# Kernel tuning notes

Hardware: AMD Instinct MI355X
Metric: run time of the kernel (lower is better)

The kernel has to match this reference:

```python
import jax, jax.numpy as jnp
import numpy as np

B, L, D, H = 4, 1024, 1024, 16
HD = D // H            # head dim 64
MAXP = 1024            # max_position_embeddings
NADJ = 2               # teacher layers mapped to this student layer


def setup_inputs() -> dict:
    key = jax.random.key(0)
    ks = jax.random.split(key, 6)
    return {
        "hidden_states": jax.random.normal(ks[0], (B, L, D), jnp.float32),
        "attention_mask": jnp.zeros((B, 1, 1, L), jnp.float32),
        "teacher_w": jax.random.normal(ks[1], (3, NADJ, D, D), jnp.float32) * 0.02,
        "wl_w": jax.random.normal(ks[2], (3, NADJ), jnp.float32),
        "scale_w": jnp.ones((3, D, D), jnp.float32),
        "shift_w": jnp.zeros((3, D, D), jnp.float32),
        "teacher_b": jax.random.normal(ks[3], (3, NADJ, D), jnp.float32) * 0.02,
        "wl_b": jax.random.normal(ks[4], (3, NADJ), jnp.float32),
        "scale_b": jnp.ones((3, D), jnp.float32),
        "shift_b": jnp.zeros((3, D), jnp.float32),
        "dist_emb": jax.random.normal(ks[5], (2 * MAXP - 1, HD), jnp.float32) * 0.02,
    }


def reference(hidden_states, attention_mask, teacher_w, wl_w, scale_w, shift_w,
              teacher_b, wl_b, scale_b, shift_b, dist_emb):
    # Teacher-distilled weight/bias generation (WeightGenerator/BiasGenerator):
    # student = tanh(mode-0 contraction of teacher subset with W_l) * W + B
    w = jnp.tanh(jnp.einsum('pl,ploi->poi', wl_w, teacher_w)) * scale_w + shift_w  # [3,out,in]
    b = jnp.tanh(jnp.einsum('pl,plo->po', wl_b, teacher_b)) * scale_b + shift_b    # [3,out]

    def proj(i):
        y = jnp.einsum('bld,od->blo', hidden_states, w[i]) + b[i]
        return y.reshape(B, L, H, HD).transpose(0, 2, 1, 3)  # [B,H,L,HD]

    q, k, v = proj(0), proj(1), proj(2)

    scores = jnp.einsum('bhld,bhrd->bhlr', q, k)  # [B,H,L,L]

    # relative_key_query positional bias
    dist = jnp.arange(L)[:, None] - jnp.arange(L)[None, :] + (MAXP - 1)  # [L,L]
    pe = dist_emb[dist]                                                  # [L,L,HD]
    scores = scores \
        + jnp.einsum('bhld,lrd->bhlr', q, pe) \
        + jnp.einsum('bhrd,lrd->bhlr', k, pe)

    scores = scores / np.sqrt(HD).astype(np.float32) + attention_mask
    probs = jax.nn.softmax(scores, axis=-1)  # dropout p=0.0 (eval)

    ctx = jnp.einsum('bhlr,bhrd->bhld', probs, v)
    return ctx.transpose(0, 2, 1, 3).reshape(B, L, D)
```

## Files before the change

kernel.cpp:

```cpp
#include <hip/hip_runtime.h>
#include <hip/hip_bf16.h>
#include <math.h>

#define D_  1024
#define L_  1024
#define B_  4
#define H_  16
#define HD_ 64

typedef __attribute__((ext_vector_type(4))) short short4_t;
typedef __attribute__((ext_vector_type(8))) short short8_t;
typedef __attribute__((ext_vector_type(4))) float f4;
typedef unsigned short u16;

__device__ __forceinline__ f4 MF(short8_t a, short8_t b, f4 c) {
  return __builtin_amdgcn_mfma_f32_16x16x32_bf16(a, b, c, 0, 0, 0);
}
__device__ __forceinline__ unsigned fbits(float x) { return __builtin_bit_cast(unsigned, x); }
__device__ __forceinline__ float bf2f(unsigned short u) {
  return __builtin_bit_cast(float, (unsigned)u << 16);
}
__device__ __forceinline__ unsigned pack2hi(float x, float y) {
  return (fbits(x) >> 16) | (fbits(y) & 0xFFFF0000u);
}
__device__ __forceinline__ float bfres(float x) {
  return x - __builtin_bit_cast(float, fbits(x) & 0xFFFF0000u);
}
__device__ __forceinline__ void gload16(const void* g, void* l) {
  __builtin_amdgcn_global_load_lds(
      (const __attribute__((address_space(1))) unsigned*)g,
      (__attribute__((address_space(3))) unsigned*)l, 16, 0, 0);
}
__device__ __forceinline__ short8_t ldsfragP(const char* base, int row, int ci) {
  return *(const short8_t*)(base + row * 128 + ((ci ^ (row & 7)) << 4));
}
__device__ __forceinline__ int perm32(int c) {
  return (c & ~31) | (((c >> 2) & 3) << 3) | (((c >> 4) & 1) << 2);
}

__global__ __launch_bounds__(256) void wgen_kernel(
    const float* __restrict__ tw, const float* __restrict__ wl,
    const float* __restrict__ sc, const float* __restrict__ sh,
    u16* __restrict__ whi, u16* __restrict__ wlo) {
  size_t i4 = (size_t)blockIdx.x * 256 + threadIdx.x;
  size_t e = i4 * 4;
  int p = (int)(e >> 20);
  size_t rem = e & 0xFFFFFu;
  float a0 = wl[p * 2 + 0], a1 = wl[p * 2 + 1];
  float4 t0 = *(const float4*)&tw[((size_t)(p * 2 + 0) << 20) + rem];
  float4 t1 = *(const float4*)&tw[((size_t)(p * 2 + 1) << 20) + rem];
  float4 s4 = *(const float4*)&sc[e];
  float4 h4 = *(const float4*)&sh[e];
  float4 o;
  o.x = tanhf(a0 * t0.x + a1 * t1.x) * s4.x + h4.x;
  o.y = tanhf(a0 * t0.y + a1 * t1.y) * s4.y + h4.y;
  o.z = tanhf(a0 * t0.z + a1 * t1.z) * s4.z + h4.z;
  o.w = tanhf(a0 * t0.w + a1 * t1.w) * s4.w + h4.w;
  const size_t off = (e & ~(size_t)1023) + perm32((int)(e & 1023) & 31) +
                     (((int)(e & 1023)) & ~31);
  uint2 hi; hi.x = pack2hi(o.x, o.y); hi.y = pack2hi(o.z, o.w);
  *(uint2*)&whi[off] = hi;
  uint2 lo; lo.x = pack2hi(bfres(o.x), bfres(o.y)); lo.y = pack2hi(bfres(o.z), bfres(o.w));
  *(uint2*)&wlo[off] = lo;
}

__global__ __launch_bounds__(256) void bgen_kernel(
    const float* __restrict__ tb, const float* __restrict__ wl,
    const float* __restrict__ sc, const float* __restrict__ sh,
    float* __restrict__ b_out) {
  int i = blockIdx.x * 256 + threadIdx.x;
  int p = i >> 10;
  int o = i & 1023;
  float v = tanhf(wl[p * 2 + 0] * tb[(p * 2 + 0) * D_ + o] +
                  wl[p * 2 + 1] * tb[(p * 2 + 1) * D_ + o]);
  b_out[i] = v * sc[i] + sh[i];
}

__global__ __launch_bounds__(256) void ecvt_kernel(
    const float* __restrict__ emb, u16* __restrict__ embh) {
  int i4 = blockIdx.x * 256 + threadIdx.x;
  if (i4 >= 32752) return;
  int e = i4 * 4;
  float4 v = *(const float4*)&emb[e];
  uint2 h2; h2.x = pack2hi(v.x, v.y); h2.y = pack2hi(v.z, v.w);
  int pe = (e & ~31) | perm32(e & 31);
  *(uint2*)&embh[pe] = h2;
}

__global__ __launch_bounds__(256) void proj_mfma_kernel(
    const float* __restrict__ hs,
    const u16* __restrict__ Bhp, const u16* __restrict__ Blp,
    const float* __restrict__ bias,
    u16* __restrict__ Qhi, u16* __restrict__ Qlo,
    u16* __restrict__ Khi, u16* __restrict__ Klo,
    u16* __restrict__ Vthi, u16* __restrict__ Vtlo) {
  __shared__ u16 Ah[128][32], Al[128][32], Bh[128][32], Bl[128][32];
  const int tid  = threadIdx.x;
  const int lane = tid & 63;
  const int wv   = tid >> 6;
  const int wm   = wv >> 1, wn = wv & 1;
  const int l15  = lane & 15, g = lane >> 4;

  const int bid = (blockIdx.x & 7) * 96 + (blockIdx.x >> 3);
  const int mt = bid & 31, nt = bid >> 5;
  const int m0 = mt * 128, n0 = nt * 128;

  f4 acc[4][4];
#pragma unroll
  for (int i = 0; i < 4; ++i)
#pragma unroll
    for (int j = 0; j < 4; ++j) acc[i][j] = f4{0.f, 0.f, 0.f, 0.f};

#pragma unroll 1
  for (int k0 = 0; k0 < D_; k0 += 32) {
#pragma unroll
    for (int s = 0; s < 4; ++s) {
      int q = wv * 4 + s;
      int plane = q >> 3, rowg = q & 7;
      const u16* src = (plane ? Blp : Bhp) +
                       (size_t)(n0 + rowg * 16 + (lane >> 2)) * 1024 + k0 + (lane & 3) * 8;
      u16* dst = (plane ? &Bl[0][0] : &Bh[0][0]) + rowg * 512;
      gload16(src, dst);
    }
#pragma unroll
    for (int c = 0; c < 4; ++c) {
      int f4id = tid + c * 256;
      int row = f4id >> 3, q4 = f4id & 7;
      float4 v = *(const float4*)&hs[(size_t)(m0 + row) * 1024 + k0 + q4 * 4];
      int col = (q4 & 3) * 8 + ((q4 >> 2) & 1) * 4;
      uint2 hi2; hi2.x = pack2hi(v.x, v.y); hi2.y = pack2hi(v.z, v.w);
      *(uint2*)&Ah[row][col] = hi2;
      uint2 lo2; lo2.x = pack2hi(bfres(v.x), bfres(v.y)); lo2.y = pack2hi(bfres(v.z), bfres(v.w));
      *(uint2*)&Al[row][col] = lo2;
    }
    __syncthreads();

    short8_t ah[4], al[4], bh[4], bl[4];
#pragma unroll
    for (int i = 0; i < 4; ++i) {
      ah[i] = *(const short8_t*)&Ah[wm * 64 + i * 16 + l15][g * 8];
      al[i] = *(const short8_t*)&Al[wm * 64 + i * 16 + l15][g * 8];
      bh[i] = *(const short8_t*)&Bh[wn * 64 + i * 16 + l15][g * 8];
      bl[i] = *(const short8_t*)&Bl[wn * 64 + i * 16 + l15][g * 8];
    }
#pragma unroll
    for (int mi = 0; mi < 4; ++mi)
#pragma unroll
      for (int ni = 0; ni < 4; ++ni) {
        acc[mi][ni] = MF(ah[mi], bh[ni], acc[mi][ni]);
        acc[mi][ni] = MF(ah[mi], bl[ni], acc[mi][ni]);
        acc[mi][ni] = MF(al[mi], bh[ni], acc[mi][ni]);
      }
    __syncthreads();
  }

  const int p = n0 >> 10;
  const int h0 = (n0 >> 6) & 15;
  const int nbase = n0 + wn * 64;
  float bnv[4];
#pragma unroll
  for (int ni = 0; ni < 4; ++ni) bnv[ni] = bias[nbase + ni * 16 + l15];
  float* T = (float*)&Ah[0][0];

#pragma unroll
  for (int mi = 0; mi < 4; ++mi) {
    __syncthreads();
#pragma unroll
    for (int ni = 0; ni < 4; ++ni)
#pragma unroll
      for (int r = 0; r < 4; ++r)
        T[(wm * 16 + 4 * g + r) * 132 + wn * 64 + ni * 16 + l15] =
            acc[mi][ni][r] + bnv[ni];
    __syncthreads();

    if (p < 2) {
      u16* PH = p ? Khi : Qhi;
      u16* PL = p ? Klo : Qlo;
      const int lr = tid >> 3;
      const int m = m0 + (lr >> 4) * 64 + mi * 16 + (lr & 15);
      const int bb = m >> 10, l = m & 1023;
#pragma unroll
      for (int c = 0; c < 4; ++c) {
        const int col = 4 * (tid & 7) + 32 * c;
        const int pc = perm32(col & 63) | (col & 64);
        const int hd = pc & 63, hl = col >> 6;
        float4 v = *(const float4*)&T[lr * 132 + col];
        uint2 hi; hi.x = pack2hi(v.x, v.y); hi.y = pack2hi(v.z, v.w);
        uint2 lo; lo.x = pack2hi(bfres(v.x), bfres(v.y)); lo.y = pack2hi(bfres(v.z), bfres(v.w));
        const size_t ad = ((size_t)(bb * 16 + h0 + hl) << 16) + (size_t)l * 64 + hd;
        *(uint2*)&PH[ad] = hi;
        *(uint2*)&PL[ad] = lo;
      }
    } else {
      const int col = (tid >> 3) & 31;
#pragma unroll
      for (int c = 0; c < 4; ++c) {
        const int cc = col + 32 * c;
        const int hd = cc & 63, hl = cc >> 6;
        const int mq = tid & 7;
        const int lr0 = 4 * mq;
        float vv[4];
#pragma unroll
        for (int k = 0; k < 4; ++k) vv[k] = T[(lr0 + k) * 132 + cc];
        const int m = m0 + (lr0 >> 4) * 64 + mi * 16 + (lr0 & 15);
        const int bb = m >> 10, l = m & 1023;
        const int pl = (l & ~31) | perm32(l & 31);
        uint2 hi; hi.x = pack2hi(vv[0], vv[1]); hi.y = pack2hi(vv[2], vv[3]);
        uint2 lo; lo.x = pack2hi(bfres(vv[0]), bfres(vv[1]));
        lo.y = pack2hi(bfres(vv[2]), bfres(vv[3]));
        const size_t ad = ((size_t)(bb * 16 + h0 + hl) << 16) + (size_t)hd * 1024 + pl;
        *(uint2*)&Vthi[ad] = hi;
        *(uint2*)&Vtlo[ad] = lo;
      }
    }
  }
}

#define KD_OFF 0
#define VD_OFF 32768
#define ER_OFF 49152
#define UB_OFF 81920
#define WB_OFF 115712
#define SM4_SIZE 149504

__global__ __launch_bounds__(512, 2) void attn7_kernel(
    const u16* __restrict__ Qhi, const u16* __restrict__ Qlo,
    const u16* __restrict__ Khi, const u16* __restrict__ Klo,
    const u16* __restrict__ Vthi, const u16* __restrict__ Vtlo,
    const u16* __restrict__ embh, const float* __restrict__ mask,
    float* __restrict__ out) {
  __shared__ __align__(16) char sm[SM4_SIZE];
  char* ERb = sm + ER_OFF;

  const int tid  = threadIdx.x;
  const int lane = tid & 63;
  const int wv   = tid >> 6;
  const int t    = wv >> 2;
  const int lh   = (wv >> 1) & 1;
  const int rh   = wv & 1;
  const int l15  = lane & 15;
  const int g    = lane >> 4;
  const int rsub = lane >> 3;
  const int scol = ((lane & 7) ^ (lane >> 3)) << 3;

  const int bid = (blockIdx.x & 7) * 64 + (blockIdx.x >> 3);
  const int lp = bid & 7, h = (bid >> 3) & 15, b = bid >> 7;
  const int l0 = lp * 128;
  const size_t bhoff = (size_t)(b * 16 + h) << 16;
  const float* maskp = mask + b * L_;

  u16* UBt = (u16*)(sm + UB_OFF) + t * 8448;
  u16* WBt = (u16*)(sm + WB_OFF) + t * 8448;

#pragma unroll
  for (int s = 0; s < 4; ++s) {
    const int idx = wv * 4 + s;
    const int plane = idx >> 4, rowg = idx & 15;
    const u16* src = (plane ? Qlo : Qhi) + bhoff +
                     (size_t)(l0 + rowg * 8 + rsub) * 64 + scol;
    gload16(src, ERb + (plane * 16 + rowg) * 1024);
  }
  __syncthreads();

  short8_t qfh[2][2], qfl[2][2];
#pragma unroll
  for (int nb = 0; nb < 2; ++nb)
#pragma unroll
    for (int kc = 0; kc < 2; ++kc) {
      const int row = 64 * t + 32 * lh + 16 * nb + l15;
      qfh[nb][kc] = ldsfragP(ERb,         row, 4 * kc + g);
      qfl[nb][kc] = ldsfragP(ERb + 16384, row, 4 * kc + g);
    }
  __syncthreads();

  const int pl0 = (wv * 2 + 0) >> 3, rg0 = (wv * 2 + 0) & 7;
  const int pl1 = (wv * 2 + 1) >> 3, rg1 = (wv * 2 + 1) & 7;
  const u16* kb0 = (pl0 ? Klo : Khi) + bhoff + (size_t)(rg0 * 8 + rsub) * 64 + scol;
  const u16* kb1 = (pl1 ? Klo : Khi) + bhoff + (size_t)(rg1 * 8 + rsub) * 64 + scol;
  const u16* vp0 = (pl0 ? Vtlo : Vthi) + bhoff + (size_t)(rg0 * 8 + rsub) * 1024 + scol;
  const u16* vp1 = (pl1 ? Vtlo : Vthi) + bhoff + (size_t)(rg1 * 8 + rsub) * 1024 + scol;
  const u16* ep  = embh + (size_t)(l0 + 896 + wv * 8 + rsub) * 64 + scol;
  const u16* kp0 = kb0 + 4096;
  const u16* kp1 = kb1 + 4096;
  char* const kdst0 = sm + KD_OFF + pl0 * 8192 + rg0 * 1024;
  char* const kdst1 = sm + KD_OFF + pl1 * 8192 + rg1 * 1024;
  char* const vdst0 = sm + VD_OFF + pl0 * 8192 + rg0 * 1024;
  char* const vdst1 = sm + VD_OFF + pl1 * 8192 + rg1 * 1024;

  {
    gload16(kb0, kdst0);
    gload16(kb1, kdst1);
    const int dmin0 = l0 + 960;
#pragma unroll
    for (int s = 0; s < 3; ++s) {
      const int grp = wv * 3 + s;
      const int slot = (dmin0 + grp * 8) & 255;
      gload16(embh + (size_t)(dmin0 + grp * 8 + rsub) * 64 + scol,
              ERb + slot * 128);
    }
  }

  f4 o_acc[4][2];
#pragma unroll
  for (int i = 0; i < 4; ++i)
#pragma unroll
    for (int j = 0; j < 2; ++j) o_acc[i][j] = f4{0.f, 0.f, 0.f, 0.f};
  float mrun[2] = {-3e38f, -3e38f};
  float lsum[2] = {0.f, 0.f};

#pragma unroll 2
  for (int rt = 0; rt < 16; ++rt) {
    const int r0 = rt * 64;
    const int cur = rt & 1;
    const int dmin = l0 - r0 + 960;

    __syncthreads();

    if (rt < 15) {
      char* kdn = sm + KD_OFF + (cur ^ 1) * 16384;
      gload16(kp0, kdn + pl0 * 8192 + rg0 * 1024);
      gload16(kp1, kdn + pl1 * 8192 + rg1 * 1024);
      kp0 += 4096; kp1 += 4096;
      const int slot = (dmin - 64 + wv * 8) & 255;
      gload16(ep, ERb + slot * 128);
      ep -= 4096;
    }
    gload16(vp0, vdst0);
    gload16(vp1, vdst1);
    vp0 += 64; vp1 += 64;

    float4 mk[2];
#pragma unroll
    for (int mb = 0; mb < 2; ++mb)
      mk[mb] = *(const float4*)&maskp[r0 + 32 * rh + 16 * mb + 4 * g];

    const char* kdc_h = sm + KD_OFF + cur * 16384;
    const char* kdc_l = kdc_h + 8192;

    f4 sacc[2][2];
#pragma unroll
    for (int i = 0; i < 2; ++i)
#pragma unroll
      for (int j = 0; j < 2; ++j) sacc[i][j] = f4{0.f, 0.f, 0.f, 0.f};
    short8_t khf[2][2];
    __builtin_amdgcn_s_setprio(1);
#pragma unroll
    for (int mb = 0; mb < 2; ++mb)
#pragma unroll
      for (int kc = 0; kc < 2; ++kc) {
        const int row = 32 * rh + 16 * mb + l15;
        short8_t ka = ldsfragP(kdc_h, row, 4 * kc + g);
        short8_t kl = ldsfragP(kdc_l, row, 4 * kc + g);
        khf[mb][kc] = ka;
#pragma unroll
        for (int nb = 0; nb < 2; ++nb) {
          sacc[mb][nb] = MF(ka, qfh[nb][kc], sacc[mb][nb]);
          sacc[mb][nb] = MF(ka, qfl[nb][kc], sacc[mb][nb]);
          sacc[mb][nb] = MF(kl, qfh[nb][kc], sacc[mb][nb]);
        }
      }
    __builtin_amdgcn_s_setprio(0);

#pragma unroll
    for (int s = 0; s < 3; ++s) {
      const int dblk = 16 * (2 * lh + 3 * rh + s);
      const int erow = (dmin + 64 * t + dblk + l15) & 255;
      const short8_t eb0 = ldsfragP(ERb, erow, g);
      const short8_t eb1 = ldsfragP(ERb, erow, 4 + g);
      f4 au0 = f4{0.f, 0.f, 0.f, 0.f}, au1 = f4{0.f, 0.f, 0.f, 0.f};
      au0 = MF(eb0, qfh[0][0], au0); au0 = MF(eb1, qfh[0][1], au0);
      au1 = MF(eb0, qfh[1][0], au1); au1 = MF(eb1, qfh[1][1], au1);
#pragma unroll
      for (int nb = 0; nb < 2; ++nb) {
        const f4 au = nb ? au1 : au0;
        uint2 w2; w2.x = pack2hi(au[0], au[1]); w2.y = pack2hi(au[2], au[3]);
        *(uint2*)&UBt[(32 * lh + 16 * nb + l15) * 132 + dblk + 4 * g] = w2;
      }
    }

#pragma unroll
    for (int s = 0; s < 3; ++s) {
      const int dblk = 16 * ((2 - 2 * rh) + 3 * lh + s);
      const int erow = (dmin + 64 * t + dblk + l15) & 255;
      const short8_t eb0 = ldsfragP(ERb, erow, g);
      const short8_t eb1 = ldsfragP(ERb, erow, 4 + g);
      f4 aw0 = f4{0.f, 0.f, 0.f, 0.f}, aw1 = f4{0.f, 0.f, 0.f, 0.f};
      aw0 = MF(eb0, khf[0][0], aw0); aw0 = MF(eb1, khf[0][1], aw0);
      aw1 = MF(eb0, khf[1][0], aw1); aw1 = MF(eb1, khf[1][1], aw1);
#pragma unroll
      for (int mb = 0; mb < 2; ++mb) {
        const f4 aw = mb ? aw1 : aw0;
        uint2 w2; w2.x = pack2hi(aw[0], aw[1]); w2.y = pack2hi(aw[2], aw[3]);
        *(uint2*)&WBt[(32 * rh + 16 * mb + l15) * 132 + dblk + 4 * g] = w2;
      }
    }
    __syncthreads();

    float pbuf[2][2][4];
#pragma unroll
    for (int nb = 0; nb < 2; ++nb) {
      const int lA = 32 * lh + 16 * nb + l15;
      float sv[2][4];
      float ml = -3e38f;
#pragma unroll
      for (int mb = 0; mb < 2; ++mb) {
        const int rr = 32 * rh + 16 * mb + 4 * g;
        const int dbase = lA + 63 - rr;
        const float mka[4] = {mk[mb].x, mk[mb].y, mk[mb].z, mk[mb].w};
#pragma unroll
        for (int j = 0; j < 4; ++j) {
          const float uu = bf2f(UBt[lA * 132 + dbase - j]);
          const float ww = bf2f(WBt[(rr + j) * 132 + dbase - j]);
          float s = (sacc[mb][nb][j] + uu + ww) * 0.125f + mka[j];
          sv[mb][j] = s;
          ml = fmaxf(ml, s);
        }
      }
      ml = fmaxf(ml, __shfl_xor(ml, 16));
      ml = fmaxf(ml, __shfl_xor(ml, 32));
      const bool nore = __all(ml <= mrun[nb]);
      const float mn = nore ? mrun[nb] : fmaxf(mrun[nb], ml);
      float ps = 0.f;
#pragma unroll
      for (int mb = 0; mb < 2; ++mb)
#pragma unroll
        for (int j = 0; j < 4; ++j) {
          const float pv = __expf(sv[mb][j] - mn);
          pbuf[nb][mb][j] = pv;
          ps += pv;
        }
      ps += __shfl_xor(ps, 16);
      ps += __shfl_xor(ps, 32);
      if (nore) {
        lsum[nb] += ps;
      } else {
        const float rs = __expf(mrun[nb] - mn);
        lsum[nb] = lsum[nb] * rs + ps;
        mrun[nb] = mn;
#pragma unroll
        for (int mbd = 0; mbd < 4; ++mbd) {
          o_acc[mbd][nb][0] *= rs; o_acc[mbd][nb][1] *= rs;
          o_acc[mbd][nb][2] *= rs; o_acc[mbd][nb][3] *= rs;
        }
      }
    }

    short8_t pf[2], pl_[2];
#pragma unroll
    for (int nb = 0; nb < 2; ++nb) {
      union { unsigned u[4]; short8_t v; } uh, ul;
      uh.u[0] = pack2hi(pbuf[nb][0][0], pbuf[nb][0][1]);
      uh.u[1] = pack2hi(pbuf[nb][0][2], pbuf[nb][0][3]);
      uh.u[2] = pack2hi(pbuf[nb][1][0], pbuf[nb][1][1]);
      uh.u[3] = pack2hi(pbuf[nb][1][2], pbuf[nb][1][3]);
      pf[nb] = uh.v;
      ul.u[0] = pack2hi(bfres(pbuf[nb][0][0]), bfres(pbuf[nb][0][1]));
      ul.u[1] = pack2hi(bfres(pbuf[nb][0][2]), bfres(pbuf[nb][0][3]));
      ul.u[2] = pack2hi(bfres(pbuf[nb][1][0]), bfres(pbuf[nb][1][1]));
      ul.u[3] = pack2hi(bfres(pbuf[nb][1][2]), bfres(pbuf[nb][1][3]));
      pl_[nb] = ul.v;
    }
    const char* vdc_h = sm + VD_OFF;
    const char* vdc_l = vdc_h + 8192;
    __builtin_amdgcn_s_setprio(1);
#pragma unroll
    for (int mbd = 0; mbd < 4; ++mbd) {
      short8_t vh = ldsfragP(vdc_h, 16 * mbd + l15, 4 * rh + g);
      short8_t vl = ldsfragP(vdc_l, 16 * mbd + l15, 4 * rh + g);
#pragma unroll
      for (int nb = 0; nb < 2; ++nb) {
        o_acc[mbd][nb] = MF(vh, pf[nb], o_acc[mbd][nb]);
        o_acc[mbd][nb] = MF(vh, pl_[nb], o_acc[mbd][nb]);
        o_acc[mbd][nb] = MF(vl, pf[nb], o_acc[mbd][nb]);
      }
    }
    __builtin_amdgcn_s_setprio(0);
  }

  __syncthreads();
  float* mbuf = (float*)ERb;
  float* obuf = (float*)(sm + UB_OFF);
  if (g == 0) {
#pragma unroll
    for (int nb = 0; nb < 2; ++nb) {
      mbuf[((wv * 2 + nb) * 16 + l15) * 2 + 0] = mrun[nb];
      mbuf[((wv * 2 + nb) * 16 + l15) * 2 + 1] = lsum[nb];
    }
  }
  __syncthreads();
  const int pw = wv ^ 1;
  float alpha[2], ltot[2];
#pragma unroll
  for (int nb = 0; nb < 2; ++nb) {
    float m2 = mbuf[((pw * 2 + nb) * 16 + l15) * 2 + 0];
    float s2 = mbuf[((pw * 2 + nb) * 16 + l15) * 2 + 1];
    float M = fmaxf(mrun[nb], m2);
    alpha[nb] = __expf(mrun[nb] - M);
    ltot[nb] = lsum[nb] * alpha[nb] + s2 * __expf(m2 - M);
  }
  const int pair = wv >> 1;
  if (rh == 1) {
#pragma unroll
    for (int mbd = 0; mbd < 4; ++mbd)
#pragma unroll
      for (int nb = 0; nb < 2; ++nb)
#pragma unroll
        for (int j = 0; j < 4; ++j)
          obuf[(pair * 64 + 16 * mbd + 4 * g + j) * 32 + 16 * nb + l15] =
              o_acc[mbd][nb][j] * alpha[nb];
  }
  __syncthreads();
  if (rh == 0) {
#pragma unroll
    for (int mbd = 0; mbd < 4; ++mbd)
#pragma unroll
      for (int nb = 0; nb < 2; ++nb) {
        const int lgl = l0 + 64 * t + 32 * lh + 16 * nb + l15;
        const float inv = 1.f / ltot[nb];
        float tmp[4];
#pragma unroll
        for (int j = 0; j < 4; ++j)
          tmp[j] = (o_acc[mbd][nb][j] * alpha[nb] +
                    obuf[(pair * 64 + 16 * mbd + 4 * g + j) * 32 + 16 * nb + l15]) * inv;
        float4 ov; ov.x = tmp[0]; ov.y = tmp[1]; ov.z = tmp[2]; ov.w = tmp[3];
        *(float4*)&out[(size_t)(b * L_ + lgl) * D_ + h * HD_ + 16 * mbd + 4 * g] = ov;
      }
  }
}

extern "C" void kernel_launch(void* const* d_in, const int* in_sizes, int n_in,
                              void* d_out, int out_size, void* d_ws, size_t ws_size,
                              hipStream_t stream) {
  const float* hs   = (const float*)d_in[0];
  const float* mask = (const float*)d_in[1];
  const float* tw   = (const float*)d_in[2];
  const float* wlw  = (const float*)d_in[3];
  const float* scw  = (const float*)d_in[4];
  const float* shw  = (const float*)d_in[5];
  const float* tb   = (const float*)d_in[6];
  const float* wlb  = (const float*)d_in[7];
  const float* scb  = (const float*)d_in[8];
  const float* shb  = (const float*)d_in[9];
  const float* emb  = (const float*)d_in[10];
  float* out = (float*)d_out;

  char* W = (char*)d_ws;
  float* b_s = (float*)W;
  u16* whi  = (u16*)(W + 12288);
  u16* wlo  = whi + 3145728;
  u16* embh = wlo + 3145728;
  u16* Qhi  = embh + 131072;
  u16* Qlo  = Qhi + 4194304;
  u16* Khi  = Qlo + 4194304;
  u16* Klo  = Khi + 4194304;
  u16* Vthi = Klo + 4194304;
  u16* Vtlo = Vthi + 4194304;

  hipLaunchKernelGGL(wgen_kernel, dim3(3072), dim3(256), 0, stream,
                     tw, wlw, scw, shw, whi, wlo);
  hipLaunchKernelGGL(bgen_kernel, dim3(12), dim3(256), 0, stream,
                     tb, wlb, scb, shb, b_s);
  hipLaunchKernelGGL(ecvt_kernel, dim3(128), dim3(256), 0, stream, emb, embh);
  hipLaunchKernelGGL(proj_mfma_kernel, dim3(768), dim3(256), 0, stream,
                     hs, whi, wlo, b_s, Qhi, Qlo, Khi, Klo, Vthi, Vtlo);
  hipLaunchKernelGGL(attn7_kernel, dim3(512), dim3(512), 0, stream,
                     Qhi, Qlo, Khi, Klo, Vthi, Vtlo, embh, mask, out);
}
```

Measured before the change: 250.4 us.

## Pre-split hidden states to bf16 hi/lo and stream via direct LDS loads

Adds a separate kernel that converts hidden_states once into permuted bf16 hi/lo planes. The projection GEMM then fetches A tiles with global_load_lds, the same way it fetches B tiles, instead of repeating the fp32 load, split and LDS store in each of the 8 n-tile blocks that share an A tile. It also replaces tanhf with an exp-based tanh in weight and bias generation. The cost is an extra launch, extra workspace traffic (16 MB written then read back), and a tanh that can lose accuracy or overflow to NaN for large inputs.

```diff
diff --git a/kernel.cpp b/kernel.cpp
--- a/kernel.cpp
+++ b/kernel.cpp
@@ -25,6 +25,10 @@
 }
 __device__ __forceinline__ float bfres(float x) {
   return x - __builtin_bit_cast(float, fbits(x) & 0xFFFF0000u);
+}
+__device__ __forceinline__ float ftanh(float x) {
+  float t = __expf(2.f * x);
+  return (t - 1.f) / (t + 1.f);
 }
 __device__ __forceinline__ void gload16(const void* g, void* l) {
   __builtin_amdgcn_global_load_lds(
@@ -52,16 +56,28 @@
   float4 s4 = *(const float4*)&sc[e];
   float4 h4 = *(const float4*)&sh[e];
   float4 o;
-  o.x = tanhf(a0 * t0.x + a1 * t1.x) * s4.x + h4.x;
-  o.y = tanhf(a0 * t0.y + a1 * t1.y) * s4.y + h4.y;
-  o.z = tanhf(a0 * t0.z + a1 * t1.z) * s4.z + h4.z;
-  o.w = tanhf(a0 * t0.w + a1 * t1.w) * s4.w + h4.w;
-  const size_t off = (e & ~(size_t)1023) + perm32((int)(e & 1023) & 31) +
-                     (((int)(e & 1023)) & ~31);
+  o.x = ftanh(a0 * t0.x + a1 * t1.x) * s4.x + h4.x;
+  o.y = ftanh(a0 * t0.y + a1 * t1.y) * s4.y + h4.y;
+  o.z = ftanh(a0 * t0.z + a1 * t1.z) * s4.z + h4.z;
+  o.w = ftanh(a0 * t0.w + a1 * t1.w) * s4.w + h4.w;
+  const size_t off = (e & ~(size_t)31) + perm32((int)(e & 31));
   uint2 hi; hi.x = pack2hi(o.x, o.y); hi.y = pack2hi(o.z, o.w);
   *(uint2*)&whi[off] = hi;
   uint2 lo; lo.x = pack2hi(bfres(o.x), bfres(o.y)); lo.y = pack2hi(bfres(o.z), bfres(o.w));
   *(uint2*)&wlo[off] = lo;
+}
+
+__global__ __launch_bounds__(256) void hscvt_kernel(
+    const float* __restrict__ hs,
+    u16* __restrict__ hhi, u16* __restrict__ hlo) {
+  size_t i4 = (size_t)blockIdx.x * 256 + threadIdx.x;
+  size_t e = i4 * 4;
+  float4 v = *(const float4*)&hs[e];
+  const size_t off = (e & ~(size_t)31) + perm32((int)(e & 31));
+  uint2 hi; hi.x = pack2hi(v.x, v.y); hi.y = pack2hi(v.z, v.w);
+  *(uint2*)&hhi[off] = hi;
+  uint2 lo; lo.x = pack2hi(bfres(v.x), bfres(v.y)); lo.y = pack2hi(bfres(v.z), bfres(v.w));
+  *(uint2*)&hlo[off] = lo;
 }
 
 __global__ __launch_bounds__(256) void bgen_kernel(
@@ -71,7 +87,7 @@
   int i = blockIdx.x * 256 + threadIdx.x;
   int p = i >> 10;
   int o = i & 1023;
-  float v = tanhf(wl[p * 2 + 0] * tb[(p * 2 + 0) * D_ + o] +
+  float v = ftanh(wl[p * 2 + 0] * tb[(p * 2 + 0) * D_ + o] +
                   wl[p * 2 + 1] * tb[(p * 2 + 1) * D_ + o]);
   b_out[i] = v * sc[i] + sh[i];
 }
@@ -88,7 +104,7 @@
 }
 
 __global__ __launch_bounds__(256) void proj_mfma_kernel(
-    const float* __restrict__ hs,
+    const u16* __restrict__ Ahp, const u16* __restrict__ Alp,
     const u16* __restrict__ Bhp, const u16* __restrict__ Blp,
     const float* __restrict__ bias,
     u16* __restrict__ Qhi, u16* __restrict__ Qlo,
@@ -111,27 +127,23 @@
 #pragma unroll
     for (int j = 0; j < 4; ++j) acc[i][j] = f4{0.f, 0.f, 0.f, 0.f};
 
+  const int srow = lane >> 2;
+  const int sck  = (lane & 3) * 8;
+
 #pragma unroll 1
   for (int k0 = 0; k0 < D_; k0 += 32) {
 #pragma unroll
-    for (int s = 0; s < 4; ++s) {
-      int q = wv * 4 + s;
-      int plane = q >> 3, rowg = q & 7;
-      const u16* src = (plane ? Blp : Bhp) +
-                       (size_t)(n0 + rowg * 16 + (lane >> 2)) * 1024 + k0 + (lane & 3) * 8;
-      u16* dst = (plane ? &Bl[0][0] : &Bh[0][0]) + rowg * 512;
+    for (int s = 0; s < 8; ++s) {
+      const int q = wv * 8 + s;
+      const int mat   = q >> 4;
+      const int plane = (q >> 3) & 1;
+      const int rowg  = q & 7;
+      const u16* base = mat ? (plane ? Alp : Ahp) : (plane ? Blp : Bhp);
+      const int  rb   = mat ? m0 : n0;
+      const u16* src = base + (size_t)(rb + rowg * 16 + srow) * 1024 + k0 + sck;
+      u16* dst = (mat ? (plane ? &Al[0][0] : &Ah[0][0])
+                      : (plane ? &Bl[0][0] : &Bh[0][0])) + rowg * 512;
       gload16(src, dst);
-    }
-#pragma unroll
-    for (int c = 0; c < 4; ++c) {
-      int f4id = tid + c * 256;
-      int row = f4id >> 3, q4 = f4id & 7;
-      float4 v = *(const float4*)&hs[(size_t)(m0 + row) * 1024 + k0 + q4 * 4];
-      int col = (q4 & 3) * 8 + ((q4 >> 2) & 1) * 4;
-      uint2 hi2; hi2.x = pack2hi(v.x, v.y); hi2.y = pack2hi(v.z, v.w);
-      *(uint2*)&Ah[row][col] = hi2;
-      uint2 lo2; lo2.x = pack2hi(bfres(v.x), bfres(v.y)); lo2.y = pack2hi(bfres(v.z), bfres(v.w));
-      *(uint2*)&Al[row][col] = lo2;
     }
     __syncthreads();
 
@@ -555,14 +567,18 @@
   u16* Klo  = Khi + 4194304;
   u16* Vthi = Klo + 4194304;
   u16* Vtlo = Vthi + 4194304;
+  u16* hhi  = Vtlo + 4194304;
+  u16* hlo  = hhi + 4194304;
 
   hipLaunchKernelGGL(wgen_kernel, dim3(3072), dim3(256), 0, stream,
                      tw, wlw, scw, shw, whi, wlo);
+  hipLaunchKernelGGL(hscvt_kernel, dim3(4096), dim3(256), 0, stream,
+                     hs, hhi, hlo);
   hipLaunchKernelGGL(bgen_kernel, dim3(12), dim3(256), 0, stream,
                      tb, wlb, scb, shb, b_s);
   hipLaunchKernelGGL(ecvt_kernel, dim3(128), dim3(256), 0, stream, emb, embh);
   hipLaunchKernelGGL(proj_mfma_kernel, dim3(768), dim3(256), 0, stream,
-                     hs, whi, wlo, b_s, Qhi, Qlo, Khi, Klo, Vthi, Vtlo);
+                     hhi, hlo, whi, wlo, b_s, Qhi, Qlo, Khi, Klo, Vthi, Vtlo);
   hipLaunchKernelGGL(attn7_kernel, dim3(512), dim3(512), 0, stream,
                      Qhi, Qlo, Khi, Klo, Vthi, Vtlo, embh, mask, out);
 }
```

After: 251.1 us. About the same (+0.3%).
